# Kernel optimization log

Hardware: AMD Instinct MI355X
Metric: run time of the kernel (lower is better)

The kernel has to match this reference:

```python
import jax, jax.numpy as jnp
import numpy as np
from jax import lax

EPS = 1e-5
INPLANES = 256


def setup_inputs() -> dict:
    key = jax.random.key(0)
    ks = jax.random.split(key, 7)
    C = INPLANES
    C2 = C // 2
    x = jax.random.normal(ks[0], (4, C, 128, 128), dtype=jnp.float32)
    s = 1.0 / np.sqrt(C)
    theta_w = jax.random.normal(ks[1], (C2, C), dtype=jnp.float32) * s
    phi_w = jax.random.normal(ks[2], (C2, C), dtype=jnp.float32) * s
    g_w = jax.random.normal(ks[3], (C2, C), dtype=jnp.float32) * s
    y_w = jax.random.normal(ks[4], (C, C2), dtype=jnp.float32) * (1.0 / np.sqrt(C2))
    bn_weight = jax.random.normal(ks[5], (C,), dtype=jnp.float32) * 0.1
    bn_bias = jax.random.normal(ks[6], (C,), dtype=jnp.float32) * 0.1
    return {"x": x, "theta_w": theta_w, "phi_w": phi_w, "g_w": g_w,
            "y_w": y_w, "bn_weight": bn_weight, "bn_bias": bn_bias}


def reference(x, theta_w, phi_w, g_w, y_w, bn_weight, bn_bias):
    # compression: per-channel 3x3 max pool, stride 2, VALID (matches
    # F.max_pool3d(kernel=(1,3,3), stride=(1,2,2)) on a 4D tensor)
    xp = lax.reduce_window(x, -jnp.inf, lax.max,
                           (1, 1, 3, 3), (1, 1, 2, 2), 'VALID')
    B, C, H, W = xp.shape
    C2 = C // 2
    N = H * W
    residual = xp
    # 1x1 convs are channel GEMMs
    theta = jnp.einsum('oc,bchw->bohw', theta_w, xp).reshape(B, C2, N)
    phi = jnp.einsum('oc,bchw->bohw', phi_w, xp).reshape(B, C2, N)
    g = jnp.einsum('oc,bchw->bohw', g_w, xp).reshape(B, C2, N)
    theta = jnp.transpose(theta, (0, 2, 1))  # (B, N, C2)
    g = jnp.transpose(g, (0, 2, 1))          # (B, N, C2)
    # embedded-gaussian attention: (B,N,N) scores, unscaled
    f = jax.nn.softmax(jnp.einsum('bnc,bcm->bnm', theta, phi), axis=-1)
    y = jnp.einsum('bnm,bmc->bnc', f, g)     # (B, N, C2)
    # FAITHFUL to torch: raw .view of contiguous (B,N,C2) into (B,C2,H,W)
    out = y.reshape(B, C2, H, W)
    out = jnp.einsum('oc,bchw->bohw', y_w, out)
    # BatchNorm2d, training mode (biased batch variance)
    mean = jnp.mean(out, axis=(0, 2, 3), keepdims=True)
    var = jnp.var(out, axis=(0, 2, 3), keepdims=True)
    out = (out - mean) * lax.rsqrt(var + EPS)
    out = out * bn_weight[None, :, None, None] + bn_bias[None, :, None, None]
    return jax.nn.relu(out + residual)
```

## Files before the change

### kernel.cpp

```cpp
#include <hip/hip_runtime.h>

#define B_   4
#define C_   256
#define C2_  128
#define HIN  128
#define HO   63
#define NSEQ 3969
#define NPAD 4032
#define QPAD 4096
#define D_   128
#define TOT  (B_*C_*NSEQ)
#define SPLITS 3

typedef _Float16 f16x8 __attribute__((ext_vector_type(8)));
typedef short    s16x8 __attribute__((ext_vector_type(8)));
typedef float    f32x4 __attribute__((ext_vector_type(4)));
typedef unsigned short u16;
typedef u16 u16x8 __attribute__((ext_vector_type(8)));

#define MFMA16(a,b,c) __builtin_amdgcn_mfma_f32_16x16x32_f16((a),(b),(c),0,0,0)
#define MFMABF(a,b,c) __builtin_amdgcn_mfma_f32_16x16x32_bf16((a),(b),(c),0,0,0)

__device__ __forceinline__ float b2f(u16 u) {
  unsigned v = ((unsigned)u) << 16;
  return __builtin_bit_cast(float, v);
}
__device__ __forceinline__ u16 f2b(float f) {
  unsigned u = __builtin_bit_cast(unsigned, f);
  return (u16)((u + 0x7FFFu + ((u >> 16) & 1u)) >> 16);
}

template<int CTRL>
__device__ __forceinline__ float dppf(float x) {
  return __builtin_bit_cast(float,
      __builtin_amdgcn_mov_dpp(__builtin_bit_cast(int, x), CTRL, 0xF, 0xF, true));
}
__device__ __forceinline__ float rmax16(float x) {
  x = fmaxf(x, dppf<0xB1>(x));
  x = fmaxf(x, dppf<0x4E>(x));
  x = fmaxf(x, dppf<0x124>(x));
  x = fmaxf(x, dppf<0x128>(x));
  return x;
}
__device__ __forceinline__ float rsum16(float x) {
  x += dppf<0xB1>(x);
  x += dppf<0x4E>(x);
  x += dppf<0x124>(x);
  x += dppf<0x128>(x);
  return x;
}

__global__ __launch_bounds__(256) void pool_k(
    const float* __restrict__ x, float* __restrict__ xp, u16* __restrict__ xpT2,
    u16* __restrict__ W2, const float* __restrict__ tw, const float* __restrict__ pw,
    const float* __restrict__ gw, float* gsum, float* gsq) {
  __shared__ unsigned Tls[64 * 69];
  int h = blockIdx.x, cg = blockIdx.y, b = blockIdx.z;
  int tid = threadIdx.x;
  if (cg == 4) {
    if (h == 0 && b == 0) { gsum[tid] = 0.f; gsq[tid] = 0.f; }
    int base = ((b * 63 + h) * 256 + tid) * 2;
#pragma unroll
    for (int e2 = 0; e2 < 2; e2++) {
      int e = base + e2;
      if (e < 3 * 128 * 256) {
        int mat = e >> 15, idx = e & 32767;
        int oc = idx >> 8, k = idx & 255;
        const float* W = (mat == 0) ? tw : (mat == 1) ? pw : gw;
        float v = W[oc * 256 + k];
        u16 hi = f2b(v);
        u16 lo = f2b(v - b2f(hi));
        W2[((long)(mat * 128 + oc)) * 512 + 2 * k]     = hi;
        W2[((long)(mat * 128 + oc)) * 512 + 2 * k + 1] = lo;
      }
    }
    return;
  }
  int cl = tid >> 2, w0 = (tid & 3) << 4;
  int c = cg * 64 + cl;
  long rowbase = ((long)(b * C_ + c) * HIN + 2 * h) * HIN + 2 * w0;
  float best[16];
#pragma unroll
  for (int j = 0; j < 16; j++) best[j] = -3e38f;
#pragma unroll
  for (int dh = 0; dh < 3; dh++) {
    long ro = rowbase + dh * HIN;
    float v[40];
#pragma unroll
    for (int ch = 0; ch < 10; ch++) {
      f32x4 a = *(const f32x4*)(x + ro + ch * 4);
#pragma unroll
      for (int j = 0; j < 4; j++) v[ch * 4 + j] = a[j];
    }
#pragma unroll
    for (int j = 0; j < 16; j++)
      best[j] = fmaxf(best[j], fmaxf(fmaxf(v[2 * j], v[2 * j + 1]), v[2 * j + 2]));
  }
  long xo = (long)(b * C_ + c) * NPAD + h * HO + w0;
#pragma unroll
  for (int j = 0; j < 16; j++)
    if (w0 + j < HO) xp[xo + j] = best[j];
#pragma unroll
  for (int j = 0; j < 16; j++) {
    u16 hi = f2b(best[j]);
    u16 lo = f2b(best[j] - b2f(hi));
    Tls[cl * 69 + w0 + j] = (unsigned)hi | ((unsigned)lo << 16);
  }
  __syncthreads();
  int w = tid >> 2, cc0 = (tid & 3) << 4;
  if (w < HO) {
    int p = h * HO + w;
    u16 outv[32];
#pragma unroll
    for (int j = 0; j < 16; j++) {
      unsigned word = Tls[(cc0 + j) * 69 + w];
      outv[2 * j]     = (u16)(word & 0xFFFF);
      outv[2 * j + 1] = (u16)(word >> 16);
    }
    u16* d = xpT2 + ((long)b * NPAD + p) * 512 + 2 * (cg * 64 + cc0);
#pragma unroll
    for (int q = 0; q < 4; q++)
      *(u16x8*)(d + q * 8) = *(u16x8*)&outv[q * 8];
  }
}

__global__ __launch_bounds__(256) void qkv_k(
    const u16* __restrict__ xpT2, const u16* __restrict__ W2,
    _Float16* Qh, _Float16* Ql, _Float16* Kv, _Float16* Vt) {
  __shared__ u16 Asm[64 * 256];
  __shared__ u16 Bsm[64 * 256];
  __shared__ float Tsm[4][16][64];
  int pt = blockIdx.x, y = blockIdx.y, b = blockIdx.z;
  int tid = threadIdx.x, wave = tid >> 6, lane = tid & 63;
  int quad = lane >> 4, l16 = lane & 15;
  int mat = y >> 1, half = y & 1;
  const u16* Wr = W2 + ((long)(mat * 128 + half * 64)) * 512;
  const u16* Xb = xpT2 + ((long)b * NPAD + pt * 64) * 512;
  f32x4 acc[4];
#pragma unroll
  for (int s = 0; s < 4; s++) acc[s] = (f32x4){0.f, 0.f, 0.f, 0.f};
#pragma unroll
  for (int ck = 0; ck < 2; ck++) {
    if (ck) __syncthreads();
#pragma unroll
    for (int i = 0; i < 8; i++) {
      int g = tid + i * 256;
      int r = g >> 5, ccc = g & 31;
      int sw = (ccc ^ (r & 15)) << 3;
      *(u16x8*)&Asm[r * 256 + sw] = *(const u16x8*)(Wr + (long)r * 512 + ck * 256 + ccc * 8);
      *(u16x8*)&Bsm[r * 256 + sw] = *(const u16x8*)(Xb + (long)r * 512 + ck * 256 + ccc * 8);
    }
    __syncthreads();
#pragma unroll
    for (int kc = 0; kc < 8; kc++) {
      s16x8 a = *(const s16x8*)&Asm[(wave * 16 + l16) * 256 + (((kc * 4 + quad) ^ l16) << 3)];
#pragma unroll
      for (int s = 0; s < 4; s++) {
        s16x8 bv = *(const s16x8*)&Bsm[(s * 16 + l16) * 256 + (((kc * 4 + quad) ^ l16) << 3)];
        acc[s] = MFMABF(a, bv, acc[s]);
      }
    }
  }
  int chanb = half * 64 + wave * 16;
  if (mat == 2) {
    _Float16* dv = Vt + (long)b * C2_ * NPAD;
#pragma unroll
    for (int s = 0; s < 4; s++)
#pragma unroll
      for (int r = 0; r < 4; r++) {
        int p = pt * 64 + s * 16 + l16;
        if (p < NSEQ) dv[(long)(chanb + quad * 4 + r) * NPAD + p] = (_Float16)acc[s][r];
      }
  } else {
#pragma unroll
    for (int s = 0; s < 4; s++)
#pragma unroll
      for (int r = 0; r < 4; r++)
        Tsm[wave][quad * 4 + r][s * 16 + l16] = acc[s][r];
    int p = pt * 64 + lane;
    if (p < NSEQ) {
      f16x8 hv[2], lv[2];
#pragma unroll
      for (int cl2 = 0; cl2 < 16; cl2++) {
        float v = Tsm[wave][cl2][lane];
        _Float16 hx = (_Float16)v;
        hv[cl2 >> 3][cl2 & 7] = hx;
        lv[cl2 >> 3][cl2 & 7] = (_Float16)(v - (float)hx);
      }
      if (mat == 0) {
        _Float16* dh = Qh + ((long)b * QPAD + p) * 128 + chanb;
        _Float16* dl = Ql + ((long)b * QPAD + p) * 128 + chanb;
        *(f16x8*)dh = hv[0]; *(f16x8*)(dh + 8) = hv[1];
        *(f16x8*)dl = lv[0]; *(f16x8*)(dl + 8) = lv[1];
      } else {
        _Float16* dk = Kv + ((long)b * NPAD + p) * 128 + chanb;
        *(f16x8*)dk = hv[0]; *(f16x8*)(dk + 8) = hv[1];
      }
    }
  }
}

__global__ __launch_bounds__(256, 3) void flash_k(
    const _Float16* __restrict__ Qh, const _Float16* __restrict__ Ql,
    const _Float16* __restrict__ Kv, const _Float16* __restrict__ Vt,
    float* __restrict__ Opart, float* __restrict__ Mp, float* __restrict__ Lp) {
  __shared__ _Float16 Ks[64 * 128];
  __shared__ _Float16 Vs[128 * 64];
  int qt = blockIdx.x, split = blockIdx.y, b = blockIdx.z;
  int tid = threadIdx.x, wave = tid >> 6, lane = tid & 63;
  int quad = lane >> 4, l16 = lane & 15;
  const _Float16* Qhb = Qh + (long)b * QPAD * D_;
  const _Float16* Qlb = Ql + (long)b * QPAD * D_;
  const _Float16* Kb  = Kv + (long)b * NPAD * D_;
  const _Float16* Vb  = Vt + (long)b * C2_ * NPAD;

  long qrow = qt * 64 + wave * 16 + l16;
  f16x8 aqh[4], aql[4];
#pragma unroll
  for (int kk = 0; kk < 4; kk++) {
    aqh[kk] = *(const f16x8*)(Qhb + qrow * D_ + kk * 32 + quad * 8);
    aql[kk] = *(const f16x8*)(Qlb + qrow * D_ + kk * 32 + quad * 8);
  }
  f32x4 o_acc[8];
#pragma unroll
  for (int s = 0; s < 8; s++) o_acc[s] = (f32x4){0.f, 0.f, 0.f, 0.f};
  float m_r[4] = {-3e38f, -3e38f, -3e38f, -3e38f};
  float l_r[4] = {0.f, 0.f, 0.f, 0.f};
  const float LOG2E = 1.4426950408889634f;
  int po = wave * 1024;

  int t0 = split * 21, t1 = t0 + 21;
  for (int t = t0; t < t1; t++) {
    __syncthreads();
#pragma unroll
    for (int i = 0; i < 4; i++) {
      int g = tid + i * 256;
      int r = g >> 4, q = g & 15;
      *(f16x8*)&Ks[r * 128 + ((q ^ (r & 15)) << 3)] =
          *(const f16x8*)(Kb + (long)(t * 64 + r) * D_ + q * 8);
      int c = g >> 3, q8 = g & 7;
      *(f16x8*)&Vs[c * 64 + ((q8 ^ (c & 7)) << 3)] =
          *(const f16x8*)(Vb + (long)c * NPAD + t * 64 + q8 * 8);
    }
    __syncthreads();

    f32x4 s_acc[4];
#pragma unroll
    for (int s = 0; s < 4; s++) s_acc[s] = (f32x4){0.f, 0.f, 0.f, 0.f};
#pragma unroll
    for (int kk = 0; kk < 4; kk++) {
      f16x8 bh[4];
#pragma unroll
      for (int s = 0; s < 4; s++)
        bh[s] = *(const f16x8*)&Ks[(s * 16 + l16) * 128 + (((kk * 4 + quad) ^ l16) << 3)];
#pragma unroll
      for (int s = 0; s < 4; s++) s_acc[s] = MFMA16(aqh[kk], bh[s], s_acc[s]);
#pragma unroll
      for (int s = 0; s < 4; s++) s_acc[s] = MFMA16(aql[kk], bh[s], s_acc[s]);
    }
    __syncthreads();

#pragma unroll
    for (int s = 0; s < 4; s++) {
      if (t * 64 + s * 16 + l16 >= NSEQ) {
#pragma unroll
        for (int r = 0; r < 4; r++) s_acc[s][r] = -3e38f;
      }
    }
    float mx[4];
#pragma unroll
    for (int r = 0; r < 4; r++) {
      mx[r] = fmaxf(fmaxf(s_acc[0][r], s_acc[1][r]), fmaxf(s_acc[2][r], s_acc[3][r]));
      mx[r] = rmax16(mx[r]);
    }
    float alpha[4];
#pragma unroll
    for (int r = 0; r < 4; r++) {
      float mn = fmaxf(m_r[r], mx[r]);
      alpha[r] = exp2f((m_r[r] - mn) * LOG2E);
      m_r[r] = mn;
    }
    float pvv[4][4], rs[4] = {0.f, 0.f, 0.f, 0.f};
#pragma unroll
    for (int s = 0; s < 4; s++)
#pragma unroll
      for (int r = 0; r < 4; r++) {
        float p = exp2f((s_acc[s][r] - m_r[r]) * LOG2E);
        pvv[s][r] = p;
        rs[r] += p;
      }
#pragma unroll
    for (int r = 0; r < 4; r++) {
      rs[r] = rsum16(rs[r]);
      l_r[r] = l_r[r] * alpha[r] + rs[r];
    }
#pragma unroll
    for (int s8 = 0; s8 < 8; s8++)
#pragma unroll
      for (int r = 0; r < 4; r++) o_acc[s8][r] *= alpha[r];
#pragma unroll
    for (int s = 0; s < 4; s++)
#pragma unroll
      for (int r = 0; r < 4; r++) {
        int m = quad * 4 + r;
        Ks[po + m * 64 + (((s * 2 + (l16 >> 3)) ^ (m & 7)) << 3) + (l16 & 7)] =
            (_Float16)pvv[s][r];
      }
    f16x8 ap[2];
#pragma unroll
    for (int kk2 = 0; kk2 < 2; kk2++)
      ap[kk2] = *(const f16x8*)&Ks[po + l16 * 64 + (((kk2 * 4 + quad) ^ (l16 & 7)) << 3)];
#pragma unroll
    for (int kk2 = 0; kk2 < 2; kk2++)
#pragma unroll
      for (int s8 = 0; s8 < 8; s8++) {
        int c2 = s8 * 16 + l16;
        f16x8 bv = *(const f16x8*)&Vs[c2 * 64 + (((kk2 * 4 + quad) ^ (c2 & 7)) << 3)];
        o_acc[s8] = MFMA16(ap[kk2], bv, o_acc[s8]);
      }
  }
  float* Ob = Opart + (long)(b * SPLITS + split) * NSEQ * D_;
  float* Mb = Mp + (long)(b * SPLITS + split) * NSEQ;
  float* Lb = Lp + (long)(b * SPLITS + split) * NSEQ;
#pragma unroll
  for (int r = 0; r < 4; r++) {
    int n = qt * 64 + wave * 16 + quad * 4 + r;
    if (n < NSEQ) {
#pragma unroll
      for (int s8 = 0; s8 < 8; s8++)
        Ob[(long)n * D_ + s8 * 16 + l16] = o_acc[s8][r];
      if (l16 == 0) { Mb[n] = m_r[r]; Lb[n] = l_r[r]; }
    }
  }
}

__global__ __launch_bounds__(256) void merge_k(const float* __restrict__ Opart,
                                               const float* __restrict__ Mp,
                                               const float* __restrict__ Lp,
                                               float* __restrict__ Y) {
  int row = blockIdx.x * 4 + (threadIdx.x >> 6);
  int lane = threadIdx.x & 63;
  int b = row / NSEQ, n = row - b * NSEQ;
  const float LOG2E = 1.4426950408889634f;
  float ms[SPLITS], m = -3e38f;
#pragma unroll
  for (int s = 0; s < SPLITS; s++) {
    ms[s] = Mp[(long)(b * SPLITS + s) * NSEQ + n];
    m = fmaxf(m, ms[s]);
  }
  float den = 0.f, a0 = 0.f, a1 = 0.f;
  int d = lane * 2;
#pragma unroll
  for (int s = 0; s < SPLITS; s++) {
    float w = exp2f((ms[s] - m) * LOG2E);
    den += Lp[(long)(b * SPLITS + s) * NSEQ + n] * w;
    const float* O = Opart + ((long)(b * SPLITS + s) * NSEQ + n) * D_ + d;
    a0 += w * O[0];
    a1 += w * O[1];
  }
  float inv = 1.f / den;
  float* Yo = Y + ((long)b * NSEQ + n) * D_ + d;
  Yo[0] = a0 * inv;
  Yo[1] = a1 * inv;
}

__global__ __launch_bounds__(256) void out_k(const float* __restrict__ Y,
                                             const float* __restrict__ yw, float* outp,
                                             float* gsum, float* gsumsq) {
  int b = blockIdx.z, ot = blockIdx.y, pb = blockIdx.x, tid = threadIdx.x;
  __shared__ float Wt[C2_][16];
  __shared__ float red[2][16][4];
#pragma unroll
  for (int i = 0; i < 8; i++) {
    int g = tid + i * 256;
    int r = g >> 7, c = g & 127;
    Wt[c][r] = yw[(ot * 16 + r) * C2_ + c];
  }
  __syncthreads();
  int p0 = pb * 512 + tid;
  const float* Yb = Y + (long)b * NSEQ * D_;
  bool val[2];
#pragma unroll
  for (int j = 0; j < 2; j++) val[j] = (p0 + j * 256) < NSEQ;
  float acc[16][2];
#pragma unroll
  for (int r = 0; r < 16; r++)
#pragma unroll
    for (int j = 0; j < 2; j++) acc[r][j] = 0.f;
  for (int c = 0; c < C2_; c++) {
    float xv[2];
#pragma unroll
    for (int j = 0; j < 2; j++) xv[j] = val[j] ? Yb[(long)c * NSEQ + p0 + j * 256] : 0.f;
#pragma unroll
    for (int r4 = 0; r4 < 4; r4++) {
      f32x4 w4 = *(const f32x4*)&Wt[c][r4 * 4];
#pragma unroll
      for (int rr = 0; rr < 4; rr++)
#pragma unroll
        for (int j = 0; j < 2; j++) acc[r4 * 4 + rr][j] += w4[rr] * xv[j];
    }
  }
  long ob = ((long)b * C_ + ot * 16) * NSEQ;
#pragma unroll
  for (int r = 0; r < 16; r++)
#pragma unroll
    for (int j = 0; j < 2; j++)
      if (val[j]) outp[ob + (long)r * NSEQ + p0 + j * 256] = acc[r][j];
  int wave = tid >> 6, lane = tid & 63;
#pragma unroll
  for (int r = 0; r < 16; r++) {
    float s = 0.f, q = 0.f;
#pragma unroll
    for (int j = 0; j < 2; j++) { s += acc[r][j]; q += acc[r][j] * acc[r][j]; }
#pragma unroll
    for (int off = 1; off < 64; off <<= 1) {
      s += __shfl_xor(s, off, 64);
      q += __shfl_xor(q, off, 64);
    }
    if (lane == 0) { red[0][r][wave] = s; red[1][r][wave] = q; }
  }
  __syncthreads();
  if (tid < 32) {
    int which = tid >> 4, r = tid & 15;
    float v = red[which][r][0] + red[which][r][1] + red[which][r][2] + red[which][r][3];
    atomicAdd((which ? gsumsq : gsum) + ot * 16 + r, v);
  }
}

__global__ __launch_bounds__(256) void bn_k(const float* __restrict__ outp,
                                            const float* gsum, const float* gsumsq,
                                            const float* __restrict__ bnw,
                                            const float* __restrict__ bnb,
                                            const float* __restrict__ xp, float* out) {
  int idx = blockIdx.x * 256 + threadIdx.x;
  if (idx >= TOT) return;
  int p = idx % NSEQ;
  int bc = idx / NSEQ;
  int c = bc & (C_ - 1);
  const float invn = 1.0f / (float)(B_ * NSEQ);
  float mean = gsum[c] * invn;
  float var = gsumsq[c] * invn - mean * mean;
  var = fmaxf(var, 0.f);
  float is = rsqrtf(var + 1e-5f);
  float v = (outp[idx] - mean) * is * bnw[c] + bnb[c] + xp[(long)bc * NPAD + p];
  out[idx] = fmaxf(v, 0.f);
}

extern "C" void kernel_launch(void* const* d_in, const int* in_sizes, int n_in,
                              void* d_out, int out_size, void* d_ws, size_t ws_size,
                              hipStream_t stream) {
  size_t off = 0;
  auto alloc = [&](size_t bytes) -> char* {
    char* p = (char*)d_ws + off;
    off += (bytes + 255) & ~(size_t)255;
    return p;
  };
  float*    xp   = (float*)alloc(sizeof(float) * (size_t)B_ * C_ * NPAD);
  u16*      xpT2 = (u16*)alloc(2 * (size_t)B_ * NPAD * 512);
  u16*      W2   = (u16*)alloc(2 * (size_t)3 * 128 * 512);
  _Float16* Qh   = (_Float16*)alloc(2 * (size_t)B_ * QPAD * D_);
  _Float16* Ql   = (_Float16*)alloc(2 * (size_t)B_ * QPAD * D_);
  _Float16* Kv   = (_Float16*)alloc(2 * (size_t)B_ * NPAD * D_);
  _Float16* Vt   = (_Float16*)alloc(2 * (size_t)B_ * C2_ * NPAD);
  float*    big  = (float*)alloc(sizeof(float) * (size_t)B_ * SPLITS * NSEQ * D_);
  float*    gsum = (float*)alloc(1024);
  float*    gsq  = (float*)alloc(1024);

  float* Mp = (float*)xpT2;
  float* Lp = Mp + (size_t)B_ * SPLITS * NSEQ;
  float* Yb = (float*)Qh;

  const float* xin = (const float*)d_in[0];
  pool_k<<<dim3(63, 5, B_), 256, 0, stream>>>(xin, xp, xpT2, W2,
                                              (const float*)d_in[1], (const float*)d_in[2],
                                              (const float*)d_in[3], gsum, gsq);
  qkv_k<<<dim3(63, 6, B_), 256, 0, stream>>>(xpT2, W2, Qh, Ql, Kv, Vt);
  flash_k<<<dim3(63, SPLITS, B_), 256, 0, stream>>>(Qh, Ql, Kv, Vt, big, Mp, Lp);
  merge_k<<<3969, 256, 0, stream>>>(big, Mp, Lp, Yb);
  out_k<<<dim3(8, 16, B_), 256, 0, stream>>>(Yb, (const float*)d_in[4], big, gsum, gsq);
  bn_k<<<(TOT + 255) / 256, 256, 0, stream>>>(big, gsum, gsq,
                                              (const float*)d_in[5], (const float*)d_in[6],
                                              xp, (float*)d_out);
}
```

Baseline: 309.6 us.

## Register-prefetch next K/V tile, separate P buffer, lazy softmax rescale, MFMA priority

```diff
diff --git a/kernel.cpp b/kernel.cpp
--- a/kernel.cpp
+++ b/kernel.cpp
@@ -206,6 +206,7 @@
     float* __restrict__ Opart, float* __restrict__ Mp, float* __restrict__ Lp) {
   __shared__ _Float16 Ks[64 * 128];
   __shared__ _Float16 Vs[128 * 64];
+  __shared__ _Float16 Ps[4 * 1024];
   int qt = blockIdx.x, split = blockIdx.y, b = blockIdx.z;
   int tid = threadIdx.x, wave = tid >> 6, lane = tid & 63;
   int quad = lane >> 4, l16 = lane & 15;
@@ -228,25 +229,39 @@
   float l_r[4] = {0.f, 0.f, 0.f, 0.f};
   const float LOG2E = 1.4426950408889634f;
   int po = wave * 1024;
-
   int t0 = split * 21, t1 = t0 + 21;
-  for (int t = t0; t < t1; t++) {
-    __syncthreads();
+
+  f16x8 kA[4], vA[4], kB[4], vB[4];
+
+  auto issue = [&](int t, f16x8 (&kr)[4], f16x8 (&vr)[4]) {
 #pragma unroll
     for (int i = 0; i < 4; i++) {
       int g = tid + i * 256;
       int r = g >> 4, q = g & 15;
-      *(f16x8*)&Ks[r * 128 + ((q ^ (r & 15)) << 3)] =
-          *(const f16x8*)(Kb + (long)(t * 64 + r) * D_ + q * 8);
+      kr[i] = *(const f16x8*)(Kb + (long)(t * 64 + r) * D_ + q * 8);
       int c = g >> 3, q8 = g & 7;
-      *(f16x8*)&Vs[c * 64 + ((q8 ^ (c & 7)) << 3)] =
-          *(const f16x8*)(Vb + (long)c * NPAD + t * 64 + q8 * 8);
-    }
+      vr[i] = *(const f16x8*)(Vb + (long)c * NPAD + t * 64 + q8 * 8);
+    }
+  };
+
+  auto body = [&](int t, f16x8 (&kr)[4], f16x8 (&vr)[4],
+                  f16x8 (&kn)[4], f16x8 (&vn)[4]) {
     __syncthreads();
+#pragma unroll
+    for (int i = 0; i < 4; i++) {
+      int g = tid + i * 256;
+      int r = g >> 4, q = g & 15;
+      *(f16x8*)&Ks[r * 128 + ((q ^ (r & 15)) << 3)] = kr[i];
+      int c = g >> 3, q8 = g & 7;
+      *(f16x8*)&Vs[c * 64 + ((q8 ^ (c & 7)) << 3)] = vr[i];
+    }
+    if (t + 1 < t1) issue(t + 1, kn, vn);
+    __syncthreads();
 
     f32x4 s_acc[4];
 #pragma unroll
     for (int s = 0; s < 4; s++) s_acc[s] = (f32x4){0.f, 0.f, 0.f, 0.f};
+    __builtin_amdgcn_s_setprio(1);
 #pragma unroll
     for (int kk = 0; kk < 4; kk++) {
       f16x8 bh[4];
@@ -258,7 +273,7 @@
 #pragma unroll
       for (int s = 0; s < 4; s++) s_acc[s] = MFMA16(aql[kk], bh[s], s_acc[s]);
     }
-    __syncthreads();
+    __builtin_amdgcn_s_setprio(0);
 
 #pragma unroll
     for (int s = 0; s < 4; s++) {
@@ -273,43 +288,44 @@
       mx[r] = fmaxf(fmaxf(s_acc[0][r], s_acc[1][r]), fmaxf(s_acc[2][r], s_acc[3][r]));
       mx[r] = rmax16(mx[r]);
     }
-    float alpha[4];
-#pragma unroll
-    for (int r = 0; r < 4; r++) {
-      float mn = fmaxf(m_r[r], mx[r]);
-      alpha[r] = exp2f((m_r[r] - mn) * LOG2E);
-      m_r[r] = mn;
-    }
-    float pvv[4][4], rs[4] = {0.f, 0.f, 0.f, 0.f};
+    bool need = false;
+#pragma unroll
+    for (int r = 0; r < 4; r++) need = need || (mx[r] > m_r[r] + 8.0f);
+    if (__any(need)) {
+      float alpha[4];
+#pragma unroll
+      for (int r = 0; r < 4; r++) {
+        float mn = fmaxf(m_r[r], mx[r]);
+        alpha[r] = exp2f((m_r[r] - mn) * LOG2E);
+        m_r[r] = mn;
+        l_r[r] *= alpha[r];
+      }
+#pragma unroll
+      for (int s8 = 0; s8 < 8; s8++)
+#pragma unroll
+        for (int r = 0; r < 4; r++) o_acc[s8][r] *= alpha[r];
+    }
+    float rs[4] = {0.f, 0.f, 0.f, 0.f};
 #pragma unroll
     for (int s = 0; s < 4; s++)
 #pragma unroll
       for (int r = 0; r < 4; r++) {
         float p = exp2f((s_acc[s][r] - m_r[r]) * LOG2E);
-        pvv[s][r] = p;
         rs[r] += p;
+        int m = quad * 4 + r;
+        Ps[po + m * 64 + (((s * 2 + (l16 >> 3)) ^ (m & 7)) << 3) + (l16 & 7)] =
+            (_Float16)p;
       }
 #pragma unroll
     for (int r = 0; r < 4; r++) {
       rs[r] = rsum16(rs[r]);
-      l_r[r] = l_r[r] * alpha[r] + rs[r];
-    }
-#pragma unroll
-    for (int s8 = 0; s8 < 8; s8++)
-#pragma unroll
-      for (int r = 0; r < 4; r++) o_acc[s8][r] *= alpha[r];
-#pragma unroll
-    for (int s = 0; s < 4; s++)
-#pragma unroll
-      for (int r = 0; r < 4; r++) {
-        int m = quad * 4 + r;
-        Ks[po + m * 64 + (((s * 2 + (l16 >> 3)) ^ (m & 7)) << 3) + (l16 & 7)] =
-            (_Float16)pvv[s][r];
-      }
+      l_r[r] += rs[r];
+    }
     f16x8 ap[2];
 #pragma unroll
     for (int kk2 = 0; kk2 < 2; kk2++)
-      ap[kk2] = *(const f16x8*)&Ks[po + l16 * 64 + (((kk2 * 4 + quad) ^ (l16 & 7)) << 3)];
+      ap[kk2] = *(const f16x8*)&Ps[po + l16 * 64 + (((kk2 * 4 + quad) ^ (l16 & 7)) << 3)];
+    __builtin_amdgcn_s_setprio(1);
 #pragma unroll
     for (int kk2 = 0; kk2 < 2; kk2++)
 #pragma unroll
@@ -318,7 +334,16 @@
         f16x8 bv = *(const f16x8*)&Vs[c2 * 64 + (((kk2 * 4 + quad) ^ (c2 & 7)) << 3)];
         o_acc[s8] = MFMA16(ap[kk2], bv, o_acc[s8]);
       }
-  }
+    __builtin_amdgcn_s_setprio(0);
+  };
+
+  issue(t0, kA, vA);
+#pragma unroll 1
+  for (int tt = 0; tt < 21; tt += 2) {
+    body(t0 + tt, kA, vA, kB, vB);
+    if (tt + 1 < 21) body(t0 + tt + 1, kB, vB, kA, vA);
+  }
+
   float* Ob = Opart + (long)(b * SPLITS + split) * NSEQ * D_;
   float* Mb = Mp + (long)(b * SPLITS + split) * NSEQ;
   float* Lb = Lp + (long)(b * SPLITS + split) * NSEQ;
```

New measurement: 429.1 us. 1.39x slower.
